# Kernel tuning notes

Hardware: AMD Instinct MI355X
Metric: run time of the kernel (lower is better)

## Reference

```python
import jax, jax.numpy as jnp
import numpy as np

VOCAB = 32000
E = 512      # embed_dim
H = 512      # hidden_dim (== embed_dim, required by the output-averaging slice)
NUM_LAYERS = 2
WIN = 8
S = 512      # seq_len
B = 8        # batch


def setup_inputs() -> dict:
    key = jax.random.key(0)
    ks = jax.random.split(key, 40)
    d = {"encoder_input": jax.random.randint(ks[0], (S, B), 0, VOCAB, dtype=jnp.int64
                                             if jax.config.jax_enable_x64 else jnp.int32)}
    d["embed_table"] = jax.random.normal(ks[1], (VOCAB, E), jnp.float32) * 0.02
    i = 2
    for l in range(NUM_LAYERS):
        in_dim = E if l == 0 else 2 * H
        for dirn in ("f", "b"):
            sc = 1.0 / np.sqrt(H).astype(np.float32)
            d[f"wih{l}{dirn}"] = jax.random.normal(ks[i], (4 * H, in_dim), jnp.float32) * sc; i += 1
            d[f"whh{l}{dirn}"] = jax.random.normal(ks[i], (4 * H, H), jnp.float32) * sc; i += 1
            d[f"b{l}{dirn}"] = jax.random.normal(ks[i], (4 * H,), jnp.float32) * sc; i += 1
    return d


def _lstm_dir(x, mask, wih, whh, b, reverse):
    """One LSTM direction over padded windows. x: [L, N, in], mask: [L, N, 1].
    Masked (out-of-window) steps carry state unchanged; since invalid steps form a
    prefix in scan order (left pad for fwd, right pad for bwd-reversed), the zero
    initial state is preserved until the first valid step -> identical math to
    running the LSTM on the truncated window, as in the original per-token loop."""
    Hh = whh.shape[1]

    def step(carry, inp):
        h, c = carry
        xt, mt = inp
        g = xt @ wih.T + h @ whh.T + b                      # [N, 4H], torch gate order i,f,g,o
        i_, f_, g_, o_ = jnp.split(g, 4, axis=-1)
        c_new = jax.nn.sigmoid(f_) * c + jax.nn.sigmoid(i_) * jnp.tanh(g_)
        h_new = jax.nn.sigmoid(o_) * jnp.tanh(c_new)
        h = jnp.where(mt, h_new, h)
        c = jnp.where(mt, c_new, c)
        return (h, c), h

    N = x.shape[1]
    h0 = jnp.zeros((N, Hh), x.dtype)
    _, ys = jax.lax.scan(step, (h0, h0), (x, mask), reverse=reverse)
    return ys  # [L, N, Hh]


def _forward(encoder_input, embed_table, layer_params):
    S_, B_ = encoder_input.shape
    L = 2 * WIN + 1
    emb = embed_table[encoder_input]                         # [S, B, E]
    offs = jnp.arange(L) - WIN
    pos = jnp.arange(S_)[:, None] + offs[None, :]            # [S, L]
    valid = (pos >= 0) & (pos < S_)
    pidx = jnp.clip(pos, 0, S_ - 1)
    windows = emb[pidx]                                      # [S, L, B, E]
    x = windows.transpose(1, 0, 2, 3).reshape(L, S_ * B_, E)  # [L, N, E]
    mask = jnp.broadcast_to(valid.T[:, :, None, None], (L, S_, B_, 1)).reshape(L, S_ * B_, 1)
    for (wf, hf, bf, wb, hb, bb) in layer_params:
        yf = _lstm_dir(x, mask, wf, hf, bf, reverse=False)
        yb = _lstm_dir(x, mask, wb, hb, bb, reverse=True)
        x = jnp.concatenate([yf, yb], axis=-1)               # [L, N, 2H]
    out = x[WIN].reshape(S_, B_, 2 * H)                      # [S, B, 2H]
    return (out[:, :, :E] + out[:, :, E:]) / 2


def reference(encoder_input, embed_table,
              wih0f, whh0f, b0f, wih0b, whh0b, b0b,
              wih1f, whh1f, b1f, wih1b, whh1b, b1b):
    layer_params = [(wih0f, whh0f, b0f, wih0b, whh0b, b0b),
                    (wih1f, whh1f, b1f, wih1b, whh1b, b1b)]
    return _forward(encoder_input, embed_table, layer_params)
```

## Files before the change

### kernel.cpp

```cpp
#include <hip/hip_runtime.h>
#include <stdint.h>

typedef __bf16 bf16;
typedef __bf16 bf16x8 __attribute__((ext_vector_type(8)));
typedef __bf16 bf16x4 __attribute__((ext_vector_type(4)));
typedef float f32x4 __attribute__((ext_vector_type(4)));

#define WIN 8

__device__ __forceinline__ float sigm(float x) { return 1.0f / (1.0f + __expf(-x)); }
__device__ __forceinline__ float tanhfast(float x) { return 2.0f / (1.0f + __expf(-2.0f * x)) - 1.0f; }

__device__ __forceinline__ void gload16(const void* g, void* l) {
    __builtin_amdgcn_global_load_lds((const __attribute__((address_space(1))) void*)g,
                                     (__attribute__((address_space(3))) void*)l, 16, 0, 0);
}

struct StepArgs {
    const bf16* A1;
    const bf16* A2;
    const bf16* W;
    const float* bias;
    const bf16* P0;
    float* Cst;
    bf16* Hout;
    float* Hf32;
    const bf16* Hprev;
    int l;
    int firstStep;
};

template<int MODE>
__global__ __launch_bounds__(256, 2)
void step_pair(StepArgs fa, StepArgs ba) {
    const StepArgs a = blockIdx.z ? ba : fa;
    __shared__ alignas(16) char lds[49152];

    constexpr int SA1 = (MODE == 0) ? 512 : 1024;
    constexpr int SW  = (MODE == 2) ? 1536 : 512;
    constexpr int SH  = (MODE == 0) ? 2048 : (MODE == 1 ? 1024 : 512);
    constexpr int SHP = (MODE == 1) ? 1024 : 512;

    const int tid = threadIdx.x;
    const int w = tid >> 6;
    const int lane = tid & 63;
    const int wm = w >> 1, wn = w & 1;
    const int bx = blockIdx.x, by = blockIdx.y;
    const int rowBase = bx * 256;

    int KB;
    if (MODE == 0) KB = 16;
    else if (MODE == 1) KB = a.firstStep ? 0 : 16;
    else KB = a.firstStep ? 32 : 48;

    const int lr = lane >> 2;
    const int lcB = (lane & 3) * 8;

    const bf16* aP[4];
    const bf16* a2P[4];
#pragma unroll
    for (int j = 0; j < 4; ++j) {
        const int r = w * 64 + j * 16 + lr;
        const int n = rowBase + r;
        aP[j] = a.A1 ? (a.A1 + (size_t)n * SA1 + lcB) : (const bf16*)0;
        if (MODE == 2) a2P[j] = a.A2 ? (a.A2 + (size_t)n * 512 + lcB) : (const bf16*)0;
    }
    const bf16* bP[2];
#pragma unroll
    for (int j = 0; j < 2; ++j) {
        const int r = w * 32 + j * 16 + lr;
        int wr;
        if (MODE == 0) wr = by * 128 + r;
        else wr = ((r >> 4) & 3) * 512 + by * 32 + (r >> 6) * 16 + (r & 15);
        bP[j] = a.W + (size_t)wr * SW + lcB;
    }

    const int l15 = lane & 15, l4 = lane >> 4;
    const int aOffB = (wm * 128 + l15) * 64 + l4 * 16;
    const int bOffB = (wn * 64 + l15) * 64 + l4 * 16;

    f32x4 acc[8][4];
    const f32x4 zf = {0.f, 0.f, 0.f, 0.f};
#pragma unroll
    for (int m = 0; m < 8; ++m)
#pragma unroll
        for (int n = 0; n < 4; ++n) acc[m][n] = zf;

    auto STAGE_A = [&](char* Sd, int kt, int j) {
        const int ke = kt * 32;
        const bf16* src;
        if (MODE == 2) src = (kt < 32) ? (aP[j] + ke) : (a2P[j] + (ke - 1024));
        else src = aP[j] + ke;
        gload16(src, Sd + (w * 64 + j * 16) * 64);
    };
    auto STAGE_B = [&](char* Sd, int kt, int j) {
        gload16(bP[j] + kt * 32, Sd + 16384 + (w * 32 + j * 16) * 64);
    };

    if (KB > 0) {
#pragma unroll
        for (int j = 0; j < 4; ++j) STAGE_A(lds, 0, j);
#pragma unroll
        for (int j = 0; j < 2; ++j) STAGE_B(lds, 0, j);
        asm volatile("s_waitcnt vmcnt(0)" ::: "memory");
        __builtin_amdgcn_s_barrier();

        for (int t = 0; t < KB; ++t) {
            const int cur = t & 1;
            const char* Ab = lds + cur * 24576;
            const char* Bb = Ab + 16384;
            char* Sd = lds + (cur ^ 1) * 24576;
            const bool pf = (t + 1 < KB);
            bf16x8 af[4], bv[4];

            if (pf) { STAGE_A(Sd, t + 1, 0); STAGE_A(Sd, t + 1, 1); STAGE_B(Sd, t + 1, 0); }
#pragma unroll
            for (int i = 0; i < 4; ++i)
                af[i] = *(const bf16x8*)(Ab + aOffB + i * 1024);
#pragma unroll
            for (int n = 0; n < 4; ++n)
                bv[n] = *(const bf16x8*)(Bb + bOffB + n * 1024);
            __builtin_amdgcn_s_barrier();
            asm volatile("s_waitcnt lgkmcnt(0)" ::: "memory");
            __builtin_amdgcn_sched_barrier(0);
            __builtin_amdgcn_s_setprio(1);
#pragma unroll
            for (int i = 0; i < 4; ++i)
#pragma unroll
                for (int n = 0; n < 4; ++n)
                    acc[i][n] = __builtin_amdgcn_mfma_f32_16x16x32_bf16(af[i], bv[n], acc[i][n], 0, 0, 0);
            __builtin_amdgcn_s_setprio(0);
            __builtin_amdgcn_sched_barrier(0);
            __builtin_amdgcn_s_barrier();

            if (pf) { STAGE_A(Sd, t + 1, 2); STAGE_A(Sd, t + 1, 3); STAGE_B(Sd, t + 1, 1); }
#pragma unroll
            for (int i = 0; i < 4; ++i)
                af[i] = *(const bf16x8*)(Ab + aOffB + (4 + i) * 1024);
            __builtin_amdgcn_s_barrier();
            asm volatile("s_waitcnt lgkmcnt(0)" ::: "memory");
            __builtin_amdgcn_sched_barrier(0);
            __builtin_amdgcn_s_setprio(1);
#pragma unroll
            for (int i = 0; i < 4; ++i)
#pragma unroll
                for (int n = 0; n < 4; ++n)
                    acc[4 + i][n] = __builtin_amdgcn_mfma_f32_16x16x32_bf16(af[i], bv[n], acc[4 + i][n], 0, 0, 0);
            __builtin_amdgcn_s_setprio(0);
            __builtin_amdgcn_sched_barrier(0);
            if (pf) asm volatile("s_waitcnt vmcnt(0)" ::: "memory");
            __builtin_amdgcn_s_barrier();
        }
    }

    if (MODE == 0) {
#pragma unroll
        for (int m = 0; m < 8; ++m)
#pragma unroll
            for (int n = 0; n < 4; ++n) {
                const int col = by * 128 + wn * 64 + n * 16 + l15;
#pragma unroll
                for (int e = 0; e < 4; ++e) {
                    const int row = rowBase + wm * 128 + m * 16 + l4 * 4 + e;
                    a.Hout[(size_t)row * SH + col] = (bf16)acc[m][n][e];
                }
            }
        return;
    }

    const int u = by * 32 + wn * 16 + l15;
    const float bi = a.bias[u];
    const float bff = a.bias[512 + u];
    const float bg = a.bias[1024 + u];
    const float bo = a.bias[1536 + u];
#pragma unroll
    for (int m = 0; m < 8; ++m) {
#pragma unroll
        for (int e = 0; e < 4; ++e) {
            const int n = rowBase + wm * 128 + m * 16 + l4 * 4 + e;
            const int s = n >> 3;
            const int p = s + a.l - WIN;
            const bool valid = ((unsigned)p < 512u);
            float gi = acc[m][0][e] + bi;
            float gf = acc[m][1][e] + bff;
            float gg = acc[m][2][e] + bg;
            float go = acc[m][3][e] + bo;
            if (MODE == 1) {
                const int pc = p < 0 ? 0 : (p > 511 ? 511 : p);
                const size_t pr = (size_t)(pc * 8 + (n & 7)) * 2048;
                gi += (float)a.P0[pr + u];
                gf += (float)a.P0[pr + 512 + u];
                gg += (float)a.P0[pr + 1024 + u];
                go += (float)a.P0[pr + 1536 + u];
            }
            const float cold = a.firstStep ? 0.0f : a.Cst[(size_t)n * 512 + u];
            const float cnew = sigm(gf) * cold + sigm(gi) * tanhfast(gg);
            const float hnew = sigm(go) * tanhfast(cnew);
            float hv, cv;
            if (valid) { hv = hnew; cv = cnew; }
            else {
                hv = a.Hprev ? (float)a.Hprev[(size_t)n * SHP + u] : 0.0f;
                cv = cold;
            }
            a.Cst[(size_t)n * 512 + u] = cv;
            a.Hout[(size_t)n * SH + u] = (bf16)hv;
            if (a.Hf32) a.Hf32[(size_t)n * 512 + u] = hv;
        }
    }
}

__global__ void embed_kernel(const int* __restrict__ tok, const float* __restrict__ tbl,
                             bf16* __restrict__ X0) {
    const int n = blockIdx.x;
    const int t = tok[n];
    const float4 v = ((const float4*)(tbl + (size_t)t * 512))[threadIdx.x];
    bf16x4 o = {(bf16)v.x, (bf16)v.y, (bf16)v.z, (bf16)v.w};
    ((bf16x4*)(X0 + (size_t)n * 512))[threadIdx.x] = o;
}

__global__ void prep_kernel(const float* __restrict__ wih0f, const float* __restrict__ wih0b,
                            const float* __restrict__ whh0f, const float* __restrict__ whh0b,
                            const float* __restrict__ wih1f, const float* __restrict__ whh1f,
                            const float* __restrict__ wih1b, const float* __restrict__ whh1b,
                            bf16* __restrict__ d0, bf16* __restrict__ d1,
                            bf16* __restrict__ d2, bf16* __restrict__ d3,
                            bf16* __restrict__ d4, bf16* __restrict__ d5) {
    const int r = blockIdx.x;
    const int y = blockIdx.y;
    if (y < 4) {
        const float* s = (y == 0) ? wih0f : (y == 1) ? wih0b : (y == 2) ? whh0f : whh0b;
        bf16* d = (y == 0) ? d0 : (y == 1) ? d1 : (y == 2) ? d2 : d3;
        const int k = threadIdx.x * 2;
        const float2 v = *(const float2*)(s + (size_t)r * 512 + k);
        d[(size_t)r * 512 + k] = (bf16)v.x;
        d[(size_t)r * 512 + k + 1] = (bf16)v.y;
    } else {
        const float* wih = (y == 4) ? wih1f : wih1b;
        const float* whh = (y == 4) ? whh1f : whh1b;
        bf16* d = (y == 4) ? d4 : d5;
        for (int k = threadIdx.x; k < 1536; k += 256) {
            const float v = (k < 1024) ? wih[(size_t)r * 1024 + k] : whh[(size_t)r * 512 + (k - 1024)];
            d[(size_t)r * 1536 + k] = (bf16)v;
        }
    }
}

__global__ void combine_kernel(const float* __restrict__ hf, const float* __restrict__ hb,
                               float* __restrict__ out) {
    const int i = blockIdx.x * 256 + threadIdx.x;
    const float4 x = ((const float4*)hf)[i];
    const float4 y = ((const float4*)hb)[i];
    float4 r;
    r.x = (x.x + y.x) * 0.5f;
    r.y = (x.y + y.y) * 0.5f;
    r.z = (x.z + y.z) * 0.5f;
    r.w = (x.w + y.w) * 0.5f;
    ((float4*)out)[i] = r;
}

extern "C" void kernel_launch(void* const* d_in, const int* in_sizes, int n_in,
                              void* d_out, int out_size, void* d_ws, size_t ws_size,
                              hipStream_t stream) {
    (void)in_sizes; (void)n_in; (void)out_size;
    const int*   tok   = (const int*)d_in[0];
    const float* tbl   = (const float*)d_in[1];
    const float* wih0f = (const float*)d_in[2];
    const float* whh0f = (const float*)d_in[3];
    const float* b0f   = (const float*)d_in[4];
    const float* wih0b = (const float*)d_in[5];
    const float* whh0b = (const float*)d_in[6];
    const float* b0b   = (const float*)d_in[7];
    const float* wih1f = (const float*)d_in[8];
    const float* whh1f = (const float*)d_in[9];
    const float* b1f   = (const float*)d_in[10];
    const float* wih1b = (const float*)d_in[11];
    const float* whh1b = (const float*)d_in[12];
    const float* b1b   = (const float*)d_in[13];

    char* ws = (char*)d_ws;
    size_t off = 0;
    auto alloc = [&](size_t bytes) -> char* {
        char* p = ws + off;
        off += (bytes + 255) & ~(size_t)255;
        return p;
    };
    bf16* wih0f_b = (bf16*)alloc((size_t)2048 * 512 * 2);
    bf16* wih0b_b = (bf16*)alloc((size_t)2048 * 512 * 2);
    bf16* whh0f_b = (bf16*)alloc((size_t)2048 * 512 * 2);
    bf16* whh0b_b = (bf16*)alloc((size_t)2048 * 512 * 2);
    bf16* w1f_b   = (bf16*)alloc((size_t)2048 * 1536 * 2);
    bf16* w1b_b   = (bf16*)alloc((size_t)2048 * 1536 * 2);
    bf16* X0      = (bf16*)alloc((size_t)4096 * 512 * 2);
    bf16* P0f     = (bf16*)alloc((size_t)4096 * 2048 * 2);
    bf16* P0b     = (bf16*)alloc((size_t)4096 * 2048 * 2);
    bf16* X1      = (bf16*)alloc((size_t)17 * 4096 * 1024 * 2);
    float* c0f    = (float*)alloc((size_t)4096 * 512 * 4);
    float* c0b    = (float*)alloc((size_t)4096 * 512 * 4);
    bf16* h1f0    = (bf16*)alloc((size_t)4096 * 512 * 2);
    bf16* h1f1    = (bf16*)alloc((size_t)4096 * 512 * 2);
    bf16* h1b0    = (bf16*)alloc((size_t)4096 * 512 * 2);
    bf16* h1b1    = (bf16*)alloc((size_t)4096 * 512 * 2);
    float* hf32f  = (float*)alloc((size_t)4096 * 512 * 4);
    float* hf32b  = (float*)alloc((size_t)4096 * 512 * 4);
    if (off > ws_size) return;

    bf16* h1f[2] = {h1f0, h1f1};
    bf16* h1b[2] = {h1b0, h1b1};

    prep_kernel<<<dim3(2048, 6), 256, 0, stream>>>(wih0f, wih0b, whh0f, whh0b,
                                                   wih1f, whh1f, wih1b, whh1b,
                                                   wih0f_b, wih0b_b, whh0f_b, whh0b_b,
                                                   w1f_b, w1b_b);
    embed_kernel<<<4096, 128, 0, stream>>>(tok, tbl, X0);

    dim3 g(16, 16, 2), blk(256, 1, 1);

    {
        StepArgs f{}, b{};
        f.A1 = X0; f.W = wih0f_b; f.Hout = P0f;
        b = f; b.W = wih0b_b; b.Hout = P0b;
        step_pair<0><<<g, blk, 0, stream>>>(f, b);
    }

    const size_t SLOT = (size_t)4096 * 1024;

    for (int i = 0; i <= 16; ++i) {
        const int lf = i, lb = 16 - i;
        StepArgs f{}, b{};
        f.A1 = (lf == 0) ? (const bf16*)0 : X1 + (size_t)(lf - 1) * SLOT;
        f.W = whh0f_b; f.bias = b0f; f.P0 = P0f; f.Cst = c0f;
        f.Hout = X1 + (size_t)lf * SLOT; f.Hprev = f.A1;
        f.l = lf; f.firstStep = (lf == 0) ? 1 : 0;
        b.A1 = (lb == 16) ? (const bf16*)0 : X1 + (size_t)(lb + 1) * SLOT + 512;
        b.W = whh0b_b; b.bias = b0b; b.P0 = P0b; b.Cst = c0b;
        b.Hout = X1 + (size_t)lb * SLOT + 512; b.Hprev = b.A1;
        b.l = lb; b.firstStep = (lb == 16) ? 1 : 0;
        step_pair<1><<<g, blk, 0, stream>>>(f, b);
    }

    for (int i = 0; i <= 8; ++i) {
        const int lf = i, lb = 16 - i;
        StepArgs f{}, b{};
        f.A1 = X1 + (size_t)lf * SLOT;
        f.A2 = (i == 0) ? (const bf16*)0 : h1f[(i + 1) & 1];
        f.W = w1f_b; f.bias = b1f; f.Cst = c0f;
        f.Hout = h1f[i & 1]; f.Hf32 = (i == 8) ? hf32f : (float*)0;
        f.Hprev = f.A2;
        f.l = lf; f.firstStep = (i == 0) ? 1 : 0;
        b.A1 = X1 + (size_t)lb * SLOT;
        b.A2 = (i == 0) ? (const bf16*)0 : h1b[(i + 1) & 1];
        b.W = w1b_b; b.bias = b1b; b.Cst = c0b;
        b.Hout = h1b[i & 1]; b.Hf32 = (i == 8) ? hf32b : (float*)0;
        b.Hprev = b.A2;
        b.l = lb; b.firstStep = (i == 0) ? 1 : 0;
        step_pair<2><<<g, blk, 0, stream>>>(f, b);
    }

    combine_kernel<<<2048, 256, 0, stream>>>(hf32f, hf32b, (float*)d_out);
}
```

Before: 1.236 ms.

## Enlarge LSTM step GEMM tile to 256x256 with 4-stage swizzled LDS pipeline

Doubles the block to 512 threads and the N-tile to 256 columns (64 hidden units × 4 gates), halving grid.y. The K loop moves from a double buffer with mid-iteration barriers to a 4-deep LDS ring with vmcnt-based waits and one barrier per k-step. LDS addresses get an XOR swizzle to cut bank conflicts. The MODE 0 projection is reordered so that P0 stores the four gates of each unit side by side, letting the gate epilogue read them with one vector load. The trade-off is a 128KB LDS footprint, which limits occupancy to about one block per CU, and higher register pressure.

```diff
diff --git a/kernel.cpp b/kernel.cpp
--- a/kernel.cpp
+++ b/kernel.cpp
@@ -31,10 +31,10 @@
 };
 
 template<int MODE>
-__global__ __launch_bounds__(256, 2)
+__global__ __launch_bounds__(512, 2)
 void step_pair(StepArgs fa, StepArgs ba) {
     const StepArgs a = blockIdx.z ? ba : fa;
-    __shared__ alignas(16) char lds[49152];
+    __shared__ alignas(16) char lds[131072];
 
     constexpr int SA1 = (MODE == 0) ? 512 : 1024;
     constexpr int SW  = (MODE == 2) ? 1536 : 512;
@@ -44,40 +44,37 @@
     const int tid = threadIdx.x;
     const int w = tid >> 6;
     const int lane = tid & 63;
-    const int wm = w >> 1, wn = w & 1;
+    const int wm = w >> 2, wn = w & 3;
     const int bx = blockIdx.x, by = blockIdx.y;
     const int rowBase = bx * 256;
 
-    int KB;
-    if (MODE == 0) KB = 16;
-    else if (MODE == 1) KB = a.firstStep ? 0 : 16;
-    else KB = a.firstStep ? 32 : 48;
-
-    const int lr = lane >> 2;
-    const int lcB = (lane & 3) * 8;
-
-    const bf16* aP[4];
-    const bf16* a2P[4];
-#pragma unroll
-    for (int j = 0; j < 4; ++j) {
-        const int r = w * 64 + j * 16 + lr;
+    int H;
+    if (MODE == 0) H = 16;
+    else if (MODE == 1) H = a.firstStep ? 0 : 16;
+    else H = a.firstStep ? 32 : 48;
+
+    const int q = lane >> 2;
+    const int soff = ((lane & 3) ^ ((q ^ (q >> 2)) & 3)) * 8;
+
+    const bf16* aP[2];
+    const bf16* a2P[2];
+    const bf16* bP[2];
+#pragma unroll
+    for (int j = 0; j < 2; ++j) {
+        const int r = w * 32 + j * 16 + q;
         const int n = rowBase + r;
-        aP[j] = a.A1 ? (a.A1 + (size_t)n * SA1 + lcB) : (const bf16*)0;
-        if (MODE == 2) a2P[j] = a.A2 ? (a.A2 + (size_t)n * 512 + lcB) : (const bf16*)0;
-    }
-    const bf16* bP[2];
-#pragma unroll
-    for (int j = 0; j < 2; ++j) {
-        const int r = w * 32 + j * 16 + lr;
+        aP[j] = a.A1 ? (a.A1 + (size_t)n * SA1 + soff) : (const bf16*)0;
+        if (MODE == 2) a2P[j] = a.A2 ? (a.A2 + (size_t)n * 512 + soff) : (const bf16*)0;
         int wr;
-        if (MODE == 0) wr = by * 128 + r;
-        else wr = ((r >> 4) & 3) * 512 + by * 32 + (r >> 6) * 16 + (r & 15);
-        bP[j] = a.W + (size_t)wr * SW + lcB;
+        if (MODE == 0) wr = (r & 3) * 512 + by * 64 + (r >> 2);
+        else wr = ((r & 63) >> 4) * 512 + by * 64 + (r >> 6) * 16 + (r & 15);
+        bP[j] = a.W + (size_t)wr * SW + soff;
     }
 
     const int l15 = lane & 15, l4 = lane >> 4;
-    const int aOffB = (wm * 128 + l15) * 64 + l4 * 16;
-    const int bOffB = (wn * 64 + l15) * 64 + l4 * 16;
+    const int rkey = (l4 ^ ((l15 ^ (l15 >> 2)) & 3)) << 4;
+    const int aOff = (wm * 128 + l15) * 64 + rkey;
+    const int bOff = (wn * 64 + l15) * 64 + rkey;
 
     f32x4 acc[8][4];
     const f32x4 zf = {0.f, 0.f, 0.f, 0.f};
@@ -86,41 +83,38 @@
 #pragma unroll
         for (int n = 0; n < 4; ++n) acc[m][n] = zf;
 
-    auto STAGE_A = [&](char* Sd, int kt, int j) {
-        const int ke = kt * 32;
-        const bf16* src;
-        if (MODE == 2) src = (kt < 32) ? (aP[j] + ke) : (a2P[j] + (ke - 1024));
-        else src = aP[j] + ke;
-        gload16(src, Sd + (w * 64 + j * 16) * 64);
+    auto STAGE = [&](int h) {
+        char* Sd = lds + (h & 3) * 32768;
+        const int ke = h * 32;
+#pragma unroll
+        for (int j = 0; j < 2; ++j) {
+            const bf16* srcA;
+            if (MODE == 2) srcA = (h < 32) ? (aP[j] + ke) : (a2P[j] + (ke - 1024));
+            else srcA = aP[j] + ke;
+            gload16(srcA, Sd + (w * 32 + j * 16) * 64);
+            gload16(bP[j] + ke, Sd + 16384 + (w * 32 + j * 16) * 64);
+        }
     };
-    auto STAGE_B = [&](char* Sd, int kt, int j) {
-        gload16(bP[j] + kt * 32, Sd + 16384 + (w * 32 + j * 16) * 64);
-    };
-
-    if (KB > 0) {
-#pragma unroll
-        for (int j = 0; j < 4; ++j) STAGE_A(lds, 0, j);
-#pragma unroll
-        for (int j = 0; j < 2; ++j) STAGE_B(lds, 0, j);
-        asm volatile("s_waitcnt vmcnt(0)" ::: "memory");
+
+    if (H > 0) {
+        STAGE(0);
+        if (H > 1) STAGE(1);
+        if (H > 2) STAGE(2);
+        if (H > 2)      asm volatile("s_waitcnt vmcnt(8)" ::: "memory");
+        else if (H > 1) asm volatile("s_waitcnt vmcnt(4)" ::: "memory");
+        else            asm volatile("s_waitcnt vmcnt(0)" ::: "memory");
         __builtin_amdgcn_s_barrier();
 
-        for (int t = 0; t < KB; ++t) {
-            const int cur = t & 1;
-            const char* Ab = lds + cur * 24576;
-            const char* Bb = Ab + 16384;
-            char* Sd = lds + (cur ^ 1) * 24576;
-            const bool pf = (t + 1 < KB);
+        for (int h = 0; h < H; ++h) {
+            const char* Sl = lds + (h & 3) * 32768;
             bf16x8 af[4], bv[4];
 
-            if (pf) { STAGE_A(Sd, t + 1, 0); STAGE_A(Sd, t + 1, 1); STAGE_B(Sd, t + 1, 0); }
+#pragma unroll
+            for (int n = 0; n < 4; ++n)
+                bv[n] = *(const bf16x8*)(Sl + 16384 + bOff + n * 1024);
 #pragma unroll
             for (int i = 0; i < 4; ++i)
-                af[i] = *(const bf16x8*)(Ab + aOffB + i * 1024);
-#pragma unroll
-            for (int n = 0; n < 4; ++n)
-                bv[n] = *(const bf16x8*)(Bb + bOffB + n * 1024);
-            __builtin_amdgcn_s_barrier();
+                af[i] = *(const bf16x8*)(Sl + aOff + i * 1024);
             asm volatile("s_waitcnt lgkmcnt(0)" ::: "memory");
             __builtin_amdgcn_sched_barrier(0);
             __builtin_amdgcn_s_setprio(1);
@@ -131,13 +125,11 @@
                     acc[i][n] = __builtin_amdgcn_mfma_f32_16x16x32_bf16(af[i], bv[n], acc[i][n], 0, 0, 0);
             __builtin_amdgcn_s_setprio(0);
             __builtin_amdgcn_sched_barrier(0);
-            __builtin_amdgcn_s_barrier();
-
-            if (pf) { STAGE_A(Sd, t + 1, 2); STAGE_A(Sd, t + 1, 3); STAGE_B(Sd, t + 1, 1); }
+
+            if (h + 3 < H) STAGE(h + 3);
 #pragma unroll
             for (int i = 0; i < 4; ++i)
-                af[i] = *(const bf16x8*)(Ab + aOffB + (4 + i) * 1024);
-            __builtin_amdgcn_s_barrier();
+                af[i] = *(const bf16x8*)(Sl + aOff + (4 + i) * 1024);
             asm volatile("s_waitcnt lgkmcnt(0)" ::: "memory");
             __builtin_amdgcn_sched_barrier(0);
             __builtin_amdgcn_s_setprio(1);
@@ -148,8 +140,13 @@
                     acc[4 + i][n] = __builtin_amdgcn_mfma_f32_16x16x32_bf16(af[i], bv[n], acc[4 + i][n], 0, 0, 0);
             __builtin_amdgcn_s_setprio(0);
             __builtin_amdgcn_sched_barrier(0);
-            if (pf) asm volatile("s_waitcnt vmcnt(0)" ::: "memory");
-            __builtin_amdgcn_s_barrier();
+
+            if (h + 1 < H) {
+                if (h + 3 < H)      asm volatile("s_waitcnt vmcnt(8)" ::: "memory");
+                else if (h + 2 < H) asm volatile("s_waitcnt vmcnt(4)" ::: "memory");
+                else                asm volatile("s_waitcnt vmcnt(0)" ::: "memory");
+                __builtin_amdgcn_s_barrier();
+            }
         }
     }
 
@@ -158,7 +155,7 @@
         for (int m = 0; m < 8; ++m)
 #pragma unroll
             for (int n = 0; n < 4; ++n) {
-                const int col = by * 128 + wn * 64 + n * 16 + l15;
+                const int col = by * 256 + wn * 64 + n * 16 + l15;
 #pragma unroll
                 for (int e = 0; e < 4; ++e) {
                     const int row = rowBase + wm * 128 + m * 16 + l4 * 4 + e;
@@ -168,16 +165,27 @@
         return;
     }
 
-    const int u = by * 32 + wn * 16 + l15;
+    const int u = by * 64 + wn * 16 + l15;
     const float bi = a.bias[u];
     const float bff = a.bias[512 + u];
     const float bg = a.bias[1024 + u];
     const float bo = a.bias[1536 + u];
 #pragma unroll
     for (int m = 0; m < 8; ++m) {
+        const int n0 = rowBase + wm * 128 + m * 16 + l4 * 4;
+        bf16x4 pg[4];
+        if (MODE == 1) {
+            const int s0 = n0 >> 3;
+            int pc = s0 + a.l - WIN;
+            pc = pc < 0 ? 0 : (pc > 511 ? 511 : pc);
+            const size_t base = ((size_t)pc * 8 + (n0 & 7)) * 2048 + u * 4;
+#pragma unroll
+            for (int e = 0; e < 4; ++e)
+                pg[e] = *(const bf16x4*)(a.P0 + base + (size_t)e * 2048);
+        }
 #pragma unroll
         for (int e = 0; e < 4; ++e) {
-            const int n = rowBase + wm * 128 + m * 16 + l4 * 4 + e;
+            const int n = n0 + e;
             const int s = n >> 3;
             const int p = s + a.l - WIN;
             const bool valid = ((unsigned)p < 512u);
@@ -186,12 +194,10 @@
             float gg = acc[m][2][e] + bg;
             float go = acc[m][3][e] + bo;
             if (MODE == 1) {
-                const int pc = p < 0 ? 0 : (p > 511 ? 511 : p);
-                const size_t pr = (size_t)(pc * 8 + (n & 7)) * 2048;
-                gi += (float)a.P0[pr + u];
-                gf += (float)a.P0[pr + 512 + u];
-                gg += (float)a.P0[pr + 1024 + u];
-                go += (float)a.P0[pr + 1536 + u];
+                gi += (float)pg[e][0];
+                gf += (float)pg[e][1];
+                gg += (float)pg[e][2];
+                go += (float)pg[e][3];
             }
             const float cold = a.firstStep ? 0.0f : a.Cst[(size_t)n * 512 + u];
             const float cnew = sigm(gf) * cold + sigm(gi) * tanhfast(gg);
@@ -313,7 +319,7 @@
                                                    w1f_b, w1b_b);
     embed_kernel<<<4096, 128, 0, stream>>>(tok, tbl, X0);
 
-    dim3 g(16, 16, 2), blk(256, 1, 1);
+    dim3 g(16, 8, 2), blk(512, 1, 1);
 
     {
         StepArgs f{}, b{};
```

New measurement: 1.100 ms. 11.0% less time.
